# Performance work log

Hardware: AMD Instinct MI355X
Metric: run time of the kernel (lower is better)

## Reference

```python
import jax, jax.numpy as jnp
import numpy as np

HEADS = 16
DIM_HEAD = 64
QUERY_DIM = 1024
CONTEXT_DIM = 1024
INNER = HEADS * DIM_HEAD  # 1024


def setup_inputs() -> dict:
    key = jax.random.key(0)
    ks = jax.random.split(key, 8)
    B, NQ, NKV = 4, 1024, 4096
    x = jax.random.normal(ks[0], (B, NQ, QUERY_DIM), dtype=jnp.float32)
    context = jax.random.normal(ks[1], (B, NKV, CONTEXT_DIM), dtype=jnp.float32)
    mask = jnp.ones((B, NKV), dtype=bool)
    sim_bias = jax.random.normal(ks[2], (B, NQ, NKV), dtype=jnp.float32)
    # learned parameters (Linear weights stored as [in, out]; to_q/to_kv have no bias)
    sq = 1.0 / np.sqrt(QUERY_DIM)
    sc = 1.0 / np.sqrt(CONTEXT_DIM)
    si = 1.0 / np.sqrt(INNER)
    Wq = jax.random.uniform(ks[3], (QUERY_DIM, INNER), jnp.float32, -sq, sq)
    Wkv = jax.random.uniform(ks[4], (CONTEXT_DIM, 2 * INNER), jnp.float32, -sc, sc)
    Wo = jax.random.uniform(ks[5], (INNER, QUERY_DIM), jnp.float32, -si, si)
    bo = jax.random.uniform(ks[6], (QUERY_DIM,), jnp.float32, -si, si)
    return {"x": x, "context": context, "mask": mask, "sim_bias": sim_bias,
            "Wq": Wq, "Wkv": Wkv, "Wo": Wo, "bo": bo}


def reference(x, context, mask, sim_bias, Wq, Wkv, Wo, bo):
    B, NQ, _ = x.shape
    _, NKV, _ = context.shape
    scale = DIM_HEAD ** -0.5
    q = x @ Wq                                   # [B, NQ, INNER]
    kv = context @ Wkv                           # [B, NKV, 2*INNER]
    k, v = kv[..., :INNER], kv[..., INNER:]
    # b n (h d) -> b h n d
    q = q.reshape(B, NQ, HEADS, DIM_HEAD).transpose(0, 2, 1, 3)
    k = k.reshape(B, NKV, HEADS, DIM_HEAD).transpose(0, 2, 1, 3)
    v = v.reshape(B, NKV, HEADS, DIM_HEAD).transpose(0, 2, 1, 3)
    sim = jnp.einsum('bhid,bhjd->bhij', q, k) * scale  # [B, H, NQ, NKV]
    sim = sim + sim_bias[:, None, :, :]
    neg = -jnp.finfo(sim.dtype).max
    sim = jnp.where(mask[:, None, None, :], sim, neg)  # kv-only mask
    attn = jax.nn.softmax(sim, axis=-1)
    out = jnp.einsum('bhij,bhjd->bhid', attn, v)       # [B, H, NQ, D]
    out = out.transpose(0, 2, 1, 3).reshape(B, NQ, INNER)
    return out @ Wo + bo
```

## Files before the change

### kernel.cpp

```cpp
#include <hip/hip_runtime.h>
#include <stdint.h>

#define B_ 4
#define H_ 16
#define NQ_ 1024
#define NKV_ 4096
#define INNER_ 1024
#define LOG2E 1.4426950408889634f

typedef __attribute__((ext_vector_type(8))) short short8;
typedef __attribute__((ext_vector_type(4))) float f32x4;
typedef __attribute__((ext_vector_type(4))) int int4v;
typedef __attribute__((ext_vector_type(4))) unsigned short u16x4;
typedef unsigned short u16;
typedef unsigned int u32;

__device__ __forceinline__ u16 f2bf(float f) {
  union { float f; u32 u; } v; v.f = f;
  u32 u = v.u;
  return (u16)((u + 0x7FFFu + ((u >> 16) & 1u)) >> 16);
}

__device__ __forceinline__ u32 cvt_pk_bf16(float lo, float hi) {
  u32 r;
  asm("v_cvt_pk_bf16_f32 %0, %1, %2" : "=v"(r) : "v"(lo), "v"(hi));
  return r;
}

__device__ __forceinline__ void gload16(const void* g, void* l) {
  __builtin_amdgcn_global_load_lds((const __attribute__((address_space(1))) void*)g,
                                   (__attribute__((address_space(3))) void*)l,
                                   16, 0, 0);
}

__global__ __launch_bounds__(256) void cast_bf16_k(const float* __restrict__ src,
                                                   u16* __restrict__ dst, int n4) {
  int i = blockIdx.x * 256 + threadIdx.x;
  if (i >= n4) return;
  float4 v = ((const float4*)src)[i];
  u16x4 o = { f2bf(v.x), f2bf(v.y), f2bf(v.z), f2bf(v.w) };
  ((u16x4*)dst)[i] = o;
}

__global__ __launch_bounds__(256) void transpose_cast_k(const float* __restrict__ src,
                                                        u16* __restrict__ dst, int C) {
  __shared__ float t[64][65];
  const int ntc = C >> 6;
  const int n0 = (blockIdx.x % ntc) << 6;
  const int k0 = (blockIdx.x / ntc) << 6;
  const int r = threadIdx.x >> 4;
  const int c4 = (threadIdx.x & 15) << 2;
#pragma unroll
  for (int it = 0; it < 4; ++it) {
    float4 v = *(const float4*)(src + (size_t)(k0 + it * 16 + r) * C + n0 + c4);
    t[it * 16 + r][c4 + 0] = v.x;
    t[it * 16 + r][c4 + 1] = v.y;
    t[it * 16 + r][c4 + 2] = v.z;
    t[it * 16 + r][c4 + 3] = v.w;
  }
  __syncthreads();
#pragma unroll
  for (int it = 0; it < 4; ++it) {
    int n = it * 16 + r;
    u16x4 o = { f2bf(t[c4 + 0][n]), f2bf(t[c4 + 1][n]),
                f2bf(t[c4 + 2][n]), f2bf(t[c4 + 3][n]) };
    *(u16x4*)(dst + (size_t)(n0 + n) * 1024 + k0 + c4) = o;
  }
}

template<int BM, int BN, int EPI>
__global__ __launch_bounds__(256) void gemm_bf16_k(
    const u16* __restrict__ A, const u16* __restrict__ Bt,
    void* __restrict__ C0, const float* __restrict__ bias, int N, int K) {
  constexpr int BK = 64;
  constexpr int WM = BM / 2, WN = BN / 2, FM = WM / 16, FN = WN / 16;
  constexpr int AIT = BM * BK * 2 / 4096, BIT = BN * BK * 2 / 4096;
  __shared__ __align__(16) u16 lsA[BM * BK];
  __shared__ __align__(16) u16 lsB[BN * BK];
  const int tid = threadIdx.x;
  const int lane = tid & 63, wid = tid >> 6;
  const int g = lane >> 4, c = lane & 15;
  const int nbn = N / BN;
  const int nb = ((int)blockIdx.x & 7) * ((int)gridDim.x >> 3) + ((int)blockIdx.x >> 3);
  const int bm = nb / nbn, bn = nb - bm * nbn;
  const int wr = wid >> 1, wc = wid & 1;

  const f32x4 zero4 = {0.f, 0.f, 0.f, 0.f};
  f32x4 acc[FM][FN];
#pragma unroll
  for (int i = 0; i < FM; ++i)
#pragma unroll
    for (int j = 0; j < FN; ++j) acc[i][j] = zero4;

  const char* Ab = (const char*)A + (size_t)(bm * BM) * K * 2;
  const char* Bb = (const char*)Bt + (size_t)(bn * BN) * K * 2;

  for (int kb = 0; kb < K; kb += BK) {
    __syncthreads();
#pragma unroll
    for (int it = 0; it < AIT; ++it) {
      int o = it * 4096 + tid * 16;
      int row = o >> 7, bb = o & 127;
      gload16(Ab + (size_t)row * (K * 2) + kb * 2 + (bb ^ ((row & 7) << 4)),
              (char*)lsA + it * 4096 + wid * 1024);
    }
#pragma unroll
    for (int it = 0; it < BIT; ++it) {
      int o = it * 4096 + tid * 16;
      int row = o >> 7, bb = o & 127;
      gload16(Bb + (size_t)row * (K * 2) + kb * 2 + (bb ^ ((row & 7) << 4)),
              (char*)lsB + it * 4096 + wid * 1024);
    }
    __syncthreads();
#pragma unroll
    for (int kk = 0; kk < 2; ++kk) {
      short8 af[FM], bf[FN];
#pragma unroll
      for (int mi = 0; mi < FM; ++mi) {
        int row = wr * WM + mi * 16 + c;
        af[mi] = *(const short8*)((const char*)lsA + row * 128 +
                                  ((kk * 64 + g * 16) ^ ((c & 7) << 4)));
      }
#pragma unroll
      for (int ni = 0; ni < FN; ++ni) {
        int row = wc * WN + ni * 16 + c;
        bf[ni] = *(const short8*)((const char*)lsB + row * 128 +
                                  ((kk * 64 + g * 16) ^ ((c & 7) << 4)));
      }
#pragma unroll
      for (int mi = 0; mi < FM; ++mi)
#pragma unroll
        for (int ni = 0; ni < FN; ++ni)
          acc[mi][ni] = __builtin_amdgcn_mfma_f32_16x16x32_bf16(af[mi], bf[ni], acc[mi][ni], 0, 0, 0);
    }
  }

#pragma unroll
  for (int mi = 0; mi < FM; ++mi)
#pragma unroll
    for (int ni = 0; ni < FN; ++ni)
#pragma unroll
      for (int r = 0; r < 4; ++r) {
        int m = bm * BM + wr * WM + mi * 16 + g * 4 + r;
        int n = bn * BN + wc * WN + ni * 16 + c;
        float v = acc[mi][ni][r];
        if constexpr (EPI == 0) {
          ((u16*)C0)[(size_t)m * N + n] = f2bf(v);
        } else {
          ((float*)C0)[(size_t)m * N + n] = v + bias[n];
        }
      }
}

__device__ __forceinline__ void stage_kv(const char* Kb, const char* Vb, int kv0,
                                         u16* lsK, u16* lsV, int tid, int wid) {
  const int row = tid >> 3;
  const int bb = (tid & 7) << 4;
  const int sw = bb ^ ((row & 7) << 4);
  gload16(Kb + (size_t)(kv0 + row) * 2048 + sw, (char*)lsK + wid * 1024);
  gload16(Vb + (size_t)row * 32768 + (size_t)kv0 * 2 + sw, (char*)lsV + wid * 1024);
}

template<bool STG>
__device__ __forceinline__ void attn_chunk(
    const u16* lsKc, const u16* lsVc, u16* lsKn, u16* lsVn,
    const char* Kb, const char* Vb, const float* BpRow, int kvc,
    f32x4 (&bcur)[4], f32x4 (&bnxt)[4],
    short8 qf0, short8 qf1, f32x4 (&acc)[4],
    float& mrun, float& lrun, int tid, int wid, int g, int c) {
  const int kvn = kvc + 64;
  if constexpr (STG) stage_kv(Kb, Vb, kvn, lsKn, lsVn, tid, wid);
  __builtin_amdgcn_sched_barrier(0);
  if constexpr (STG) asm volatile("s_waitcnt vmcnt(2)" ::: "memory");
  else               asm volatile("s_waitcnt vmcnt(0)" ::: "memory");
  __builtin_amdgcn_s_barrier();
  __builtin_amdgcn_sched_barrier(0);

  const f32x4 zero4 = {0.f, 0.f, 0.f, 0.f};
  f32x4 sv[4];
  __builtin_amdgcn_s_setprio(1);
#pragma unroll
  for (int st = 0; st < 4; ++st) {
    f32x4 s = zero4;
    const char* kr = (const char*)lsKc + (st * 16 + c) * 128;
    short8 ka0 = *(const short8*)(kr + ((g * 16) ^ ((c & 7) << 4)));
    short8 ka1 = *(const short8*)(kr + ((64 + g * 16) ^ ((c & 7) << 4)));
    s = __builtin_amdgcn_mfma_f32_16x16x32_bf16(ka0, qf0, s, 0, 0, 0);
    s = __builtin_amdgcn_mfma_f32_16x16x32_bf16(ka1, qf1, s, 0, 0, 0);
    sv[st] = s;
  }
  __builtin_amdgcn_s_setprio(0);

  if constexpr (STG) {
#pragma unroll
    for (int st = 0; st < 4; ++st)
      bnxt[st] = *(const f32x4*)(BpRow + kvn + st * 16);
  }

#pragma unroll
  for (int st = 0; st < 4; ++st)
#pragma unroll
    for (int r = 0; r < 4; ++r)
      sv[st][r] = fmaf(sv[st][r], 0.125f, bcur[st][r]);

  float m01 = fmaxf(fmaxf(sv[0][0], sv[0][1]), fmaxf(sv[0][2], sv[0][3]));
  float m23 = fmaxf(fmaxf(sv[1][0], sv[1][1]), fmaxf(sv[1][2], sv[1][3]));
  float m45 = fmaxf(fmaxf(sv[2][0], sv[2][1]), fmaxf(sv[2][2], sv[2][3]));
  float m67 = fmaxf(fmaxf(sv[3][0], sv[3][1]), fmaxf(sv[3][2], sv[3][3]));
  float cm = fmaxf(fmaxf(m01, m23), fmaxf(m45, m67));
  cm = fmaxf(cm, __shfl_xor(cm, 16));
  cm = fmaxf(cm, __shfl_xor(cm, 32));

  if (!__all(cm <= mrun + 8.f)) {
    float nm = fmaxf(mrun, cm);
    float fs = __builtin_amdgcn_exp2f((mrun - nm) * LOG2E);
    mrun = nm;
    lrun *= fs;
    float fr[4];
#pragma unroll
    for (int r = 0; r < 4; ++r) fr[r] = __shfl(fs, g * 4 + r);
#pragma unroll
    for (int db = 0; db < 4; ++db)
#pragma unroll
      for (int r = 0; r < 4; ++r) acc[db][r] *= fr[r];
  }

  const float nml = mrun * LOG2E;
  u32 pk[4][2];
  float psum = 0.f;
#pragma unroll
  for (int st = 0; st < 4; ++st) {
    float p0 = __builtin_amdgcn_exp2f(fmaf(sv[st][0], LOG2E, -nml));
    float p1 = __builtin_amdgcn_exp2f(fmaf(sv[st][1], LOG2E, -nml));
    float p2 = __builtin_amdgcn_exp2f(fmaf(sv[st][2], LOG2E, -nml));
    float p3 = __builtin_amdgcn_exp2f(fmaf(sv[st][3], LOG2E, -nml));
    psum += (p0 + p1) + (p2 + p3);
    pk[st][0] = cvt_pk_bf16(p0, p1);
    pk[st][1] = cvt_pk_bf16(p2, p3);
  }
  lrun += psum;

#pragma unroll
  for (int kc = 0; kc < 2; ++kc) {
    int4v af;
#pragma unroll
    for (int w = 0; w < 4; ++w) {
      int src = ((g & 1) * 2 + (w >> 1)) * 16 + c;
      int t0 = __shfl((int)pk[kc * 2][w & 1], src);
      int t1 = __shfl((int)pk[kc * 2 + 1][w & 1], src);
      af[w] = (g >= 2) ? t1 : t0;
    }
    short8 pa = __builtin_bit_cast(short8, af);
    __builtin_amdgcn_s_setprio(1);
#pragma unroll
    for (int db = 0; db < 4; ++db) {
      short8 vf = *(const short8*)((const char*)lsVc + (db * 16 + c) * 128 +
                                   ((kc * 64 + g * 16) ^ ((c & 7) << 4)));
      acc[db] = __builtin_amdgcn_mfma_f32_16x16x32_bf16(pa, vf, acc[db], 0, 0, 0);
    }
    __builtin_amdgcn_s_setprio(0);
  }
  asm volatile("s_waitcnt lgkmcnt(0)" ::: "memory");
  __builtin_amdgcn_sched_barrier(0);
  __builtin_amdgcn_s_barrier();
}

__global__ __launch_bounds__(512, 4) void attn_k(
    const u16* __restrict__ Qp, const u16* __restrict__ Kp,
    const u16* __restrict__ Vt, const float* __restrict__ sbias,
    u16* __restrict__ Op) {
  __shared__ __align__(16) u16 lsK0[64 * 64];
  __shared__ __align__(16) u16 lsV0[64 * 64];
  __shared__ __align__(16) u16 lsK1[64 * 64];
  __shared__ __align__(16) u16 lsV1[64 * 64];
  const int tid = threadIdx.x;
  const int lane = tid & 63, wid = tid >> 6;
  const int g = lane >> 4, c = lane & 15;
  const int d0 = blockIdx.x;
  const int b = d0 >> 7;
  const int h = (d0 >> 3) & 15;
  const int qt = d0 & 7;

  const int qrow = qt * 128 + wid * 16 + c;
  const char* Qb = (const char*)Qp + ((size_t)(b * NQ_ + qrow) * INNER_ + h * 64) * 2;
  short8 qf0 = *(const short8*)(Qb + g * 16);
  short8 qf1 = *(const short8*)(Qb + 64 + g * 16);

  const char* Kb = (const char*)Kp + (size_t)b * NKV_ * 2048 + h * 128;
  const char* Vb = (const char*)Vt + (size_t)(h * 64) * (NKV_ * B_ * 2) + (size_t)b * NKV_ * 2;
  const float* BpRow = sbias + (size_t)(b * NQ_ + qrow) * NKV_ + g * 4;

  const f32x4 zero4 = {0.f, 0.f, 0.f, 0.f};
  f32x4 acc[4];
#pragma unroll
  for (int j = 0; j < 4; ++j) acc[j] = zero4;
  float mrun = -1e30f, lrun = 0.f;

  f32x4 bcur[4], bnxt[4];
  stage_kv(Kb, Vb, 0, lsK0, lsV0, tid, wid);
#pragma unroll
  for (int st = 0; st < 4; ++st) bcur[st] = *(const f32x4*)(BpRow + st * 16);

  for (int ci = 0; ci < 62; ci += 2) {
    attn_chunk<true>(lsK0, lsV0, lsK1, lsV1, Kb, Vb, BpRow, ci * 64,
                     bcur, bnxt, qf0, qf1, acc, mrun, lrun, tid, wid, g, c);
    attn_chunk<true>(lsK1, lsV1, lsK0, lsV0, Kb, Vb, BpRow, (ci + 1) * 64,
                     bnxt, bcur, qf0, qf1, acc, mrun, lrun, tid, wid, g, c);
  }
  attn_chunk<true>(lsK0, lsV0, lsK1, lsV1, Kb, Vb, BpRow, 62 * 64,
                   bcur, bnxt, qf0, qf1, acc, mrun, lrun, tid, wid, g, c);
  attn_chunk<false>(lsK1, lsV1, lsK0, lsV0, Kb, Vb, BpRow, 63 * 64,
                    bnxt, bcur, qf0, qf1, acc, mrun, lrun, tid, wid, g, c);

  float l2 = lrun + __shfl_xor(lrun, 16);
  float lt = l2 + __shfl_xor(l2, 32);
  float inv = 1.f / lt;
  float invr[4];
#pragma unroll
  for (int r = 0; r < 4; ++r) invr[r] = __shfl(inv, g * 4 + r);

  u16* Ob = Op + (size_t)(b * NQ_ + qt * 128 + wid * 16) * INNER_ + h * 64;
#pragma unroll
  for (int db = 0; db < 4; ++db)
#pragma unroll
    for (int r = 0; r < 4; ++r)
      Ob[(size_t)(g * 4 + r) * INNER_ + db * 16 + c] = f2bf(acc[db][r] * invr[r]);
}

static constexpr size_t XB_OFF   = 0;
static constexpr size_t CTXB_OFF = 8u  << 20;
static constexpr size_t WQT_OFF  = 40u << 20;
static constexpr size_t WKVT_OFF = 42u << 20;
static constexpr size_t WOT_OFF  = 46u << 20;
static constexpr size_t QP_OFF   = 48u << 20;
static constexpr size_t KP_OFF   = 56u << 20;
static constexpr size_t VT_OFF   = 88u << 20;
static constexpr size_t OP_OFF   = 120u << 20;

extern "C" void kernel_launch(void* const* d_in, const int* in_sizes, int n_in,
                              void* d_out, int out_size, void* d_ws, size_t ws_size,
                              hipStream_t stream) {
  const float* x        = (const float*)d_in[0];
  const float* context  = (const float*)d_in[1];
  const float* sim_bias = (const float*)d_in[3];
  const float* Wq       = (const float*)d_in[4];
  const float* Wkv      = (const float*)d_in[5];
  const float* Wo       = (const float*)d_in[6];
  const float* bo       = (const float*)d_in[7];

  char* ws = (char*)d_ws;
  u16* xb   = (u16*)(ws + XB_OFF);
  u16* ctxb = (u16*)(ws + CTXB_OFF);
  u16* WqT  = (u16*)(ws + WQT_OFF);
  u16* WkvT = (u16*)(ws + WKVT_OFF);
  u16* WoT  = (u16*)(ws + WOT_OFF);
  u16* Qp   = (u16*)(ws + QP_OFF);
  u16* Kp   = (u16*)(ws + KP_OFF);
  u16* VtP  = (u16*)(ws + VT_OFF);
  u16* OpB  = (u16*)(ws + OP_OFF);

  cast_bf16_k<<<(B_ * NQ_ * 1024 / 4) / 256, 256, 0, stream>>>(x, xb, B_ * NQ_ * 1024 / 4);
  cast_bf16_k<<<(B_ * NKV_ * 1024 / 4) / 256, 256, 0, stream>>>(context, ctxb, B_ * NKV_ * 1024 / 4);
  transpose_cast_k<<<(1024 / 64) * 16, 256, 0, stream>>>(Wq, WqT, 1024);
  transpose_cast_k<<<(2048 / 64) * 16, 256, 0, stream>>>(Wkv, WkvT, 2048);
  transpose_cast_k<<<(1024 / 64) * 16, 256, 0, stream>>>(Wo, WoT, 1024);

  gemm_bf16_k<128, 128, 0><<<(16384 / 128) * (1024 / 128), 256, 0, stream>>>(
      ctxb, WkvT, Kp, nullptr, 1024, 1024);
  gemm_bf16_k<128, 128, 0><<<(1024 / 128) * (16384 / 128), 256, 0, stream>>>(
      WkvT + (size_t)1024 * 1024, ctxb, VtP, nullptr, 16384, 1024);
  gemm_bf16_k<128, 128, 0><<<(4096 / 128) * (1024 / 128), 256, 0, stream>>>(
      xb, WqT, Qp, nullptr, 1024, 1024);

  attn_k<<<512, 512, 0, stream>>>(Qp, Kp, VtP, sim_bias, OpB);

  gemm_bf16_k<128, 128, 2><<<(4096 / 128) * (1024 / 128), 256, 0, stream>>>(
      OpB, WoT, d_out, bo, 1024, 1024);
}
```

Before: 486.8 us.

## Fuse prep and projection launches, triple-buffer KV in attention, defer rescale

```diff
diff --git a/kernel.cpp b/kernel.cpp
--- a/kernel.cpp
+++ b/kernel.cpp
@@ -33,26 +33,41 @@
                                    16, 0, 0);
 }
 
-__global__ __launch_bounds__(256) void cast_bf16_k(const float* __restrict__ src,
-                                                   u16* __restrict__ dst, int n4) {
-  int i = blockIdx.x * 256 + threadIdx.x;
-  if (i >= n4) return;
-  float4 v = ((const float4*)src)[i];
-  u16x4 o = { f2bf(v.x), f2bf(v.y), f2bf(v.z), f2bf(v.w) };
-  ((u16x4*)dst)[i] = o;
-}
-
-__global__ __launch_bounds__(256) void transpose_cast_k(const float* __restrict__ src,
-                                                        u16* __restrict__ dst, int C) {
+__global__ __launch_bounds__(256) void prep_k(
+    const float* __restrict__ x, const float* __restrict__ ctx,
+    const float* __restrict__ Wq, const float* __restrict__ Wkv,
+    const float* __restrict__ Wo,
+    u16* __restrict__ xb, u16* __restrict__ ctxb,
+    u16* __restrict__ WqT, u16* __restrict__ WkvT, u16* __restrict__ WoT) {
   __shared__ float t[64][65];
+  const int bid = blockIdx.x;
+  if (bid < 20480) {
+    const float* s;
+    u16* d;
+    int i0;
+    if (bid < 4096) { s = x; d = xb; i0 = bid; }
+    else            { s = ctx; d = ctxb; i0 = bid - 4096; }
+    int i = i0 * 256 + threadIdx.x;
+    float4 v = ((const float4*)s)[i];
+    u16x4 o = { f2bf(v.x), f2bf(v.y), f2bf(v.z), f2bf(v.w) };
+    ((u16x4*)d)[i] = o;
+    return;
+  }
+  int tb = bid - 20480;
+  const float* s;
+  u16* d;
+  int C, lb;
+  if (tb < 256)      { s = Wq;  d = WqT;  C = 1024; lb = tb; }
+  else if (tb < 768) { s = Wkv; d = WkvT; C = 2048; lb = tb - 256; }
+  else               { s = Wo;  d = WoT;  C = 1024; lb = tb - 768; }
   const int ntc = C >> 6;
-  const int n0 = (blockIdx.x % ntc) << 6;
-  const int k0 = (blockIdx.x / ntc) << 6;
+  const int n0 = (lb % ntc) << 6;
+  const int k0 = (lb / ntc) << 6;
   const int r = threadIdx.x >> 4;
   const int c4 = (threadIdx.x & 15) << 2;
 #pragma unroll
   for (int it = 0; it < 4; ++it) {
-    float4 v = *(const float4*)(src + (size_t)(k0 + it * 16 + r) * C + n0 + c4);
+    float4 v = *(const float4*)(s + (size_t)(k0 + it * 16 + r) * C + n0 + c4);
     t[it * 16 + r][c4 + 0] = v.x;
     t[it * 16 + r][c4 + 1] = v.y;
     t[it * 16 + r][c4 + 2] = v.z;
@@ -64,25 +79,21 @@
     int n = it * 16 + r;
     u16x4 o = { f2bf(t[c4 + 0][n]), f2bf(t[c4 + 1][n]),
                 f2bf(t[c4 + 2][n]), f2bf(t[c4 + 3][n]) };
-    *(u16x4*)(dst + (size_t)(n0 + n) * 1024 + k0 + c4) = o;
-  }
-}
-
-template<int BM, int BN, int EPI>
-__global__ __launch_bounds__(256) void gemm_bf16_k(
+    *(u16x4*)(d + (size_t)(n0 + n) * 1024 + k0 + c4) = o;
+  }
+}
+
+template<int EPI>
+__device__ __forceinline__ void gemm_body(
     const u16* __restrict__ A, const u16* __restrict__ Bt,
-    void* __restrict__ C0, const float* __restrict__ bias, int N, int K) {
-  constexpr int BK = 64;
+    void* __restrict__ C0, const float* __restrict__ bias,
+    int N, int K, int bm, int bn, u16* lsA, u16* lsB) {
+  constexpr int BM = 128, BN = 128, BK = 64;
   constexpr int WM = BM / 2, WN = BN / 2, FM = WM / 16, FN = WN / 16;
   constexpr int AIT = BM * BK * 2 / 4096, BIT = BN * BK * 2 / 4096;
-  __shared__ __align__(16) u16 lsA[BM * BK];
-  __shared__ __align__(16) u16 lsB[BN * BK];
   const int tid = threadIdx.x;
   const int lane = tid & 63, wid = tid >> 6;
   const int g = lane >> 4, c = lane & 15;
-  const int nbn = N / BN;
-  const int nb = ((int)blockIdx.x & 7) * ((int)gridDim.x >> 3) + ((int)blockIdx.x >> 3);
-  const int bm = nb / nbn, bn = nb - bm * nbn;
   const int wr = wid >> 1, wc = wid & 1;
 
   const f32x4 zero4 = {0.f, 0.f, 0.f, 0.f};
@@ -152,6 +163,37 @@
       }
 }
 
+__global__ __launch_bounds__(256) void proj_gemm_k(
+    const u16* __restrict__ ctxb, const u16* __restrict__ WkvT,
+    const u16* __restrict__ xb, const u16* __restrict__ WqT,
+    u16* __restrict__ Kp, u16* __restrict__ VtP, u16* __restrict__ Qp) {
+  __shared__ __align__(16) u16 lsA[128 * 64];
+  __shared__ __align__(16) u16 lsB[128 * 64];
+  int nb = ((int)blockIdx.x & 7) * 288 + ((int)blockIdx.x >> 3);
+  const u16 *A, *Bt;
+  u16* C;
+  int N, bm, bn;
+  if (nb < 1024) {
+    A = ctxb; Bt = WkvT; C = Kp; N = 1024; bm = nb >> 3; bn = nb & 7;
+  } else if (nb < 2048) {
+    int l = nb - 1024;
+    A = WkvT + (size_t)1024 * 1024; Bt = ctxb; C = VtP; N = 16384; bm = l >> 7; bn = l & 127;
+  } else {
+    int l = nb - 2048;
+    A = xb; Bt = WqT; C = Qp; N = 1024; bm = l >> 3; bn = l & 7;
+  }
+  gemm_body<0>(A, Bt, C, nullptr, N, 1024, bm, bn, lsA, lsB);
+}
+
+__global__ __launch_bounds__(256) void out_gemm_k(
+    const u16* __restrict__ A, const u16* __restrict__ Bt,
+    float* __restrict__ C0, const float* __restrict__ bias) {
+  __shared__ __align__(16) u16 lsA[128 * 64];
+  __shared__ __align__(16) u16 lsB[128 * 64];
+  int nb = ((int)blockIdx.x & 7) * 32 + ((int)blockIdx.x >> 3);
+  gemm_body<2>(A, Bt, C0, bias, 1024, 1024, nb >> 3, nb & 7, lsA, lsB);
+}
+
 __device__ __forceinline__ void stage_kv(const char* Kb, const char* Vb, int kv0,
                                          u16* lsK, u16* lsV, int tid, int wid) {
   const int row = tid >> 3;
@@ -161,18 +203,25 @@
   gload16(Vb + (size_t)row * 32768 + (size_t)kv0 * 2 + sw, (char*)lsV + wid * 1024);
 }
 
-template<bool STG>
+template<int VMC, bool SKV, bool SB>
 __device__ __forceinline__ void attn_chunk(
-    const u16* lsKc, const u16* lsVc, u16* lsKn, u16* lsVn,
-    const char* Kb, const char* Vb, const float* BpRow, int kvc,
-    f32x4 (&bcur)[4], f32x4 (&bnxt)[4],
+    const u16* lsKc, const u16* lsVc, u16* lsKs, u16* lsVs,
+    const char* Kb, const char* Vb, int kvs,
+    const float* BpRow, int bpf,
+    f32x4 (&bcur)[4], f32x4 (&bpre)[4],
     short8 qf0, short8 qf1, f32x4 (&acc)[4],
     float& mrun, float& lrun, int tid, int wid, int g, int c) {
-  const int kvn = kvc + 64;
-  if constexpr (STG) stage_kv(Kb, Vb, kvn, lsKn, lsVn, tid, wid);
+  if constexpr (SKV) stage_kv(Kb, Vb, kvs * 64, lsKs, lsVs, tid, wid);
+  if constexpr (SB) {
+#pragma unroll
+    for (int st = 0; st < 4; ++st)
+      bpre[st] = *(const f32x4*)(BpRow + bpf * 64 + st * 16);
+  }
   __builtin_amdgcn_sched_barrier(0);
-  if constexpr (STG) asm volatile("s_waitcnt vmcnt(2)" ::: "memory");
-  else               asm volatile("s_waitcnt vmcnt(0)" ::: "memory");
+  if constexpr (VMC == 16) asm volatile("s_waitcnt vmcnt(16)" ::: "memory");
+  else if constexpr (VMC == 14) asm volatile("s_waitcnt vmcnt(14)" ::: "memory");
+  else if constexpr (VMC == 12) asm volatile("s_waitcnt vmcnt(12)" ::: "memory");
+  else asm volatile("s_waitcnt vmcnt(8)" ::: "memory");
   __builtin_amdgcn_s_barrier();
   __builtin_amdgcn_sched_barrier(0);
 
@@ -191,39 +240,17 @@
   }
   __builtin_amdgcn_s_setprio(0);
 
-  if constexpr (STG) {
-#pragma unroll
-    for (int st = 0; st < 4; ++st)
-      bnxt[st] = *(const f32x4*)(BpRow + kvn + st * 16);
-  }
-
 #pragma unroll
   for (int st = 0; st < 4; ++st)
 #pragma unroll
     for (int r = 0; r < 4; ++r)
       sv[st][r] = fmaf(sv[st][r], 0.125f, bcur[st][r]);
 
-  float m01 = fmaxf(fmaxf(sv[0][0], sv[0][1]), fmaxf(sv[0][2], sv[0][3]));
-  float m23 = fmaxf(fmaxf(sv[1][0], sv[1][1]), fmaxf(sv[1][2], sv[1][3]));
-  float m45 = fmaxf(fmaxf(sv[2][0], sv[2][1]), fmaxf(sv[2][2], sv[2][3]));
-  float m67 = fmaxf(fmaxf(sv[3][0], sv[3][1]), fmaxf(sv[3][2], sv[3][3]));
-  float cm = fmaxf(fmaxf(m01, m23), fmaxf(m45, m67));
-  cm = fmaxf(cm, __shfl_xor(cm, 16));
-  cm = fmaxf(cm, __shfl_xor(cm, 32));
-
-  if (!__all(cm <= mrun + 8.f)) {
-    float nm = fmaxf(mrun, cm);
-    float fs = __builtin_amdgcn_exp2f((mrun - nm) * LOG2E);
-    mrun = nm;
-    lrun *= fs;
-    float fr[4];
-#pragma unroll
-    for (int r = 0; r < 4; ++r) fr[r] = __shfl(fs, g * 4 + r);
-#pragma unroll
-    for (int db = 0; db < 4; ++db)
-#pragma unroll
-      for (int r = 0; r < 4; ++r) acc[db][r] *= fr[r];
-  }
+  float cm = fmaxf(fmaxf(fmaxf(sv[0][0], sv[0][1]), sv[0][2]),
+                   fmaxf(fmaxf(sv[0][3], sv[1][0]), sv[1][1]));
+  cm = fmaxf(cm, fmaxf(fmaxf(sv[1][2], sv[1][3]), sv[2][0]));
+  cm = fmaxf(cm, fmaxf(fmaxf(sv[2][1], sv[2][2]), sv[2][3]));
+  cm = fmaxf(cm, fmaxf(fmaxf(sv[3][0], sv[3][1]), fmaxf(sv[3][2], sv[3][3])));
 
   const float nml = mrun * LOG2E;
   u32 pk[4][2];
@@ -260,6 +287,24 @@
     }
     __builtin_amdgcn_s_setprio(0);
   }
+
+  if (!__all(cm <= mrun + 8.f)) {
+    float nm = cm;
+    nm = fmaxf(nm, __shfl_xor(nm, 1));
+    nm = fmaxf(nm, __shfl_xor(nm, 2));
+    nm = fmaxf(nm, __shfl_xor(nm, 4));
+    nm = fmaxf(nm, __shfl_xor(nm, 8));
+    nm = fmaxf(nm, __shfl_xor(nm, 16));
+    nm = fmaxf(nm, __shfl_xor(nm, 32));
+    float f = __builtin_amdgcn_exp2f((mrun - nm) * LOG2E);
+    mrun = nm;
+    lrun *= f;
+#pragma unroll
+    for (int db = 0; db < 4; ++db)
+#pragma unroll
+      for (int r = 0; r < 4; ++r) acc[db][r] *= f;
+  }
+
   asm volatile("s_waitcnt lgkmcnt(0)" ::: "memory");
   __builtin_amdgcn_sched_barrier(0);
   __builtin_amdgcn_s_barrier();
@@ -269,17 +314,16 @@
     const u16* __restrict__ Qp, const u16* __restrict__ Kp,
     const u16* __restrict__ Vt, const float* __restrict__ sbias,
     u16* __restrict__ Op) {
-  __shared__ __align__(16) u16 lsK0[64 * 64];
-  __shared__ __align__(16) u16 lsV0[64 * 64];
-  __shared__ __align__(16) u16 lsK1[64 * 64];
-  __shared__ __align__(16) u16 lsV1[64 * 64];
+  __shared__ __align__(16) u16 lsK[3 * 4096];
+  __shared__ __align__(16) u16 lsV[3 * 4096];
   const int tid = threadIdx.x;
   const int lane = tid & 63, wid = tid >> 6;
   const int g = lane >> 4, c = lane & 15;
-  const int d0 = blockIdx.x;
-  const int b = d0 >> 7;
-  const int h = (d0 >> 3) & 15;
-  const int qt = d0 & 7;
+  const int idx = blockIdx.x;
+  const int xcd = idx & 7, rr = idx >> 3;
+  const int b = xcd >> 1;
+  const int h = ((xcd & 1) << 3) | (rr >> 3);
+  const int qt = rr & 7;
 
   const int qrow = qt * 128 + wid * 16 + c;
   const char* Qb = (const char*)Qp + ((size_t)(b * NQ_ + qrow) * INNER_ + h * 64) * 2;
@@ -294,23 +338,47 @@
   f32x4 acc[4];
 #pragma unroll
   for (int j = 0; j < 4; ++j) acc[j] = zero4;
-  float mrun = -1e30f, lrun = 0.f;
-
-  f32x4 bcur[4], bnxt[4];
-  stage_kv(Kb, Vb, 0, lsK0, lsV0, tid, wid);
-#pragma unroll
-  for (int st = 0; st < 4; ++st) bcur[st] = *(const f32x4*)(BpRow + st * 16);
-
-  for (int ci = 0; ci < 62; ci += 2) {
-    attn_chunk<true>(lsK0, lsV0, lsK1, lsV1, Kb, Vb, BpRow, ci * 64,
-                     bcur, bnxt, qf0, qf1, acc, mrun, lrun, tid, wid, g, c);
-    attn_chunk<true>(lsK1, lsV1, lsK0, lsV0, Kb, Vb, BpRow, (ci + 1) * 64,
-                     bnxt, bcur, qf0, qf1, acc, mrun, lrun, tid, wid, g, c);
-  }
-  attn_chunk<true>(lsK0, lsV0, lsK1, lsV1, Kb, Vb, BpRow, 62 * 64,
-                   bcur, bnxt, qf0, qf1, acc, mrun, lrun, tid, wid, g, c);
-  attn_chunk<false>(lsK1, lsV1, lsK0, lsV0, Kb, Vb, BpRow, 63 * 64,
-                    bnxt, bcur, qf0, qf1, acc, mrun, lrun, tid, wid, g, c);
+  float mrun = 0.f, lrun = 0.f;
+
+  u16* K0 = lsK, *K1 = lsK + 4096, *K2 = lsK + 8192;
+  u16* V0 = lsV, *V1 = lsV + 4096, *V2 = lsV + 8192;
+
+  f32x4 bA[4], bB[4];
+  stage_kv(Kb, Vb, 0, K0, V0, tid, wid);
+  stage_kv(Kb, Vb, 64, K1, V1, tid, wid);
+#pragma unroll
+  for (int st = 0; st < 4; ++st) bA[st] = *(const f32x4*)(BpRow + st * 16);
+
+  attn_chunk<12, true, true>(K0, V0, K2, V2, Kb, Vb, 2, BpRow, 1,
+                             bA, bB, qf0, qf1, acc, mrun, lrun, tid, wid, g, c);
+
+  int cb = 1, n = 1;
+  for (int i = 0; i < 30; ++i) {
+    {
+      u16* Kc = lsK + cb * 4096, *Vc = lsV + cb * 4096;
+      int sb = (cb == 0) ? 2 : cb - 1;
+      u16* Ks = lsK + sb * 4096, *Vs = lsV + sb * 4096;
+      attn_chunk<16, true, true>(Kc, Vc, Ks, Vs, Kb, Vb, n + 2, BpRow, n + 1,
+                                 bB, bA, qf0, qf1, acc, mrun, lrun, tid, wid, g, c);
+      cb = (cb == 2) ? 0 : cb + 1;
+      ++n;
+    }
+    {
+      u16* Kc = lsK + cb * 4096, *Vc = lsV + cb * 4096;
+      int sb = (cb == 0) ? 2 : cb - 1;
+      u16* Ks = lsK + sb * 4096, *Vs = lsV + sb * 4096;
+      attn_chunk<16, true, true>(Kc, Vc, Ks, Vs, Kb, Vb, n + 2, BpRow, n + 1,
+                                 bA, bB, qf0, qf1, acc, mrun, lrun, tid, wid, g, c);
+      cb = (cb == 2) ? 0 : cb + 1;
+      ++n;
+    }
+  }
+  attn_chunk<16, true, true>(K1, V1, K0, V0, Kb, Vb, 63, BpRow, 62,
+                             bB, bA, qf0, qf1, acc, mrun, lrun, tid, wid, g, c);
+  attn_chunk<14, false, true>(K2, V2, K0, V0, Kb, Vb, 0, BpRow, 63,
+                              bA, bB, qf0, qf1, acc, mrun, lrun, tid, wid, g, c);
+  attn_chunk<8, false, false>(K0, V0, K1, V1, Kb, Vb, 0, BpRow, 0,
+                              bB, bA, qf0, qf1, acc, mrun, lrun, tid, wid, g, c);
 
   float l2 = lrun + __shfl_xor(lrun, 16);
   float lt = l2 + __shfl_xor(l2, 32);
@@ -359,21 +427,8 @@
   u16* VtP  = (u16*)(ws + VT_OFF);
   u16* OpB  = (u16*)(ws + OP_OFF);
 
-  cast_bf16_k<<<(B_ * NQ_ * 1024 / 4) / 256, 256, 0, stream>>>(x, xb, B_ * NQ_ * 1024 / 4);
-  cast_bf16_k<<<(B_ * NKV_ * 1024 / 4) / 256, 256, 0, stream>>>(context, ctxb, B_ * NKV_ * 1024 / 4);
-  transpose_cast_k<<<(1024 / 64) * 16, 256, 0, stream>>>(Wq, WqT, 1024);
-  transpose_cast_k<<<(2048 / 64) * 16, 256, 0, stream>>>(Wkv, WkvT, 2048);
-  transpose_cast_k<<<(1024 / 64) * 16, 256, 0, stream>>>(Wo, WoT, 1024);
-
-  gemm_bf16_k<128, 128, 0><<<(16384 / 128) * (1024 / 128), 256, 0, stream>>>(
-      ctxb, WkvT, Kp, nullptr, 1024, 1024);
-  gemm_bf16_k<128, 128, 0><<<(1024 / 128) * (16384 / 128), 256, 0, stream>>>(
-      WkvT + (size_t)1024 * 1024, ctxb, VtP, nullptr, 16384, 1024);
-  gemm_bf16_k<128, 128, 0><<<(4096 / 128) * (1024 / 128), 256, 0, stream>>>(
-      xb, WqT, Qp, nullptr, 1024, 1024);
-
+  prep_k<<<21504, 256, 0, stream>>>(x, context, Wq, Wkv, Wo, xb, ctxb, WqT, WkvT, WoT);
+  proj_gemm_k<<<2304, 256, 0, stream>>>(ctxb, WkvT, xb, WqT, Kp, VtP, Qp);
   attn_k<<<512, 512, 0, stream>>>(Qp, Kp, VtP, sim_bias, OpB);
-
-  gemm_bf16_k<128, 128, 2><<<(4096 / 128) * (1024 / 128), 256, 0, stream>>>(
-      OpB, WoT, d_out, bo, 1024, 1024);
-}
+  out_gemm_k<<<256, 256, 0, stream>>>(OpB, WoT, (float*)d_out, bo);
+}
```

Result: faster. 435.1 us (-10.6%).
